# Kernel optimization log

Hardware: AMD Instinct MI355X
Metric: run time of the kernel (lower is better)

Reference implementation:

```python
import jax, jax.numpy as jnp
import numpy as np

IN_FEATURES = 4096
OUT_FEATURES = 768
N_BITS = 8
BATCH = 4096


def setup_inputs() -> dict:
    key = jax.random.key(0)
    k1, k2, k3 = jax.random.split(key, 3)
    latent = jax.random.uniform(k1, (BATCH, IN_FEATURES), dtype=jnp.float32)
    true_sum = jax.random.uniform(k2, (BATCH, OUT_FEATURES * N_BITS), dtype=jnp.float32)
    # kaiming-normal-ish init: std = sqrt(2 / fan_in)
    weight = jax.random.normal(k3, (IN_FEATURES, OUT_FEATURES * N_BITS), dtype=jnp.float32) * np.sqrt(2.0 / IN_FEATURES)
    return {"latent": latent, "true_sum": true_sum, "weight": weight, "n_bits": N_BITS}


def reference(latent, true_sum, weight, n_bits):
    in_features = weight.shape[0]
    batch = latent.shape[0]
    # powers of two, MSB negated (two's-complement style decode)
    powers = (2.0 ** jnp.arange(n_bits, dtype=jnp.float32))
    powers = powers.at[-1].multiply(-1.0)

    prob_weights = jax.nn.sigmoid(weight)                      # [in, out*n_bits]
    # decode soft bits -> integer-valued weights: [in, out]
    int_weights = (prob_weights.reshape(in_features, -1, n_bits) * powers).sum(-1)
    # decode target bits -> integer-valued sums: [batch, out]
    int_sum = (true_sum.reshape(batch, -1, n_bits) * powers).sum(-1)

    # (latent.unsqueeze(-1) * int_weights).sum(-2) is exactly a GEMM
    pred = latent @ int_weights                                # [batch, out]

    scale_factor = 2.0 ** (n_bits - 1)
    recon_loss = jnp.mean((pred - int_sum) ** 2) / scale_factor
    polarize_loss = jnp.mean(prob_weights * (1.0 - prob_weights))
    return (recon_loss, polarize_loss)
```

## Files before the change

### kernel.cpp

```cpp
#include <hip/hip_runtime.h>
#include <stdint.h>

#define IN_F   4096
#define OUT_F  768
#define NB     8
#define BATCH  4096
#define WCOLS  (OUT_F*NB)
#define PREDN  (BATCH*OUT_F)

typedef short  bf16x8  __attribute__((ext_vector_type(8)));
typedef float  f32x4   __attribute__((ext_vector_type(4)));
typedef unsigned short ushort8 __attribute__((ext_vector_type(8)));

__device__ __forceinline__ unsigned short f2bf(float f){
    union { float f; uint32_t u; } v; v.f = f;
    uint32_t u = v.u;
    u += 0x7FFFu + ((u >> 16) & 1u);
    return (unsigned short)(u >> 16);
}

__device__ __forceinline__ void gload16(const void* g, void* l){
    __builtin_amdgcn_global_load_lds(
        (const __attribute__((address_space(1))) unsigned int*)g,
        (__attribute__((address_space(3))) unsigned int*)l, 16, 0, 0);
}

#define SBAR() __builtin_amdgcn_sched_barrier(0)

__launch_bounds__(256)
__global__ void decode_all(const float* __restrict__ w,
                           const float* __restrict__ lat,
                           unsigned short* __restrict__ bt,
                           unsigned short* __restrict__ abf,
                           float* __restrict__ polp){
    __shared__ unsigned short tile[64][70];
    __shared__ float part[4];
    const int tid = threadIdx.x;
    const int bid = blockIdx.x;
    if (bid < 768){
        const int k0 = (bid & 63) * 64;
        const int n0 = (bid >> 6) * 64;
        const int j     = tid & 63;
        const int ibase = (tid >> 6) * 16;
        float pol = 0.f;
        #pragma unroll
        for (int grp = 0; grp < 4; ++grp){
            float4 va[4][2];
            #pragma unroll
            for (int r = 0; r < 4; ++r){
                int i = ibase + grp*4 + r;
                const float4* src = (const float4*)(w + (size_t)(k0+i)*WCOLS
                                                      + (size_t)(n0+j)*8);
                va[r][0] = src[0];
                va[r][1] = src[1];
            }
            SBAR();
            #pragma unroll
            for (int r = 0; r < 4; ++r){
                float x[8] = {va[r][0].x, va[r][0].y, va[r][0].z, va[r][0].w,
                              va[r][1].x, va[r][1].y, va[r][1].z, va[r][1].w};
                float p[8];
                #pragma unroll
                for (int q = 0; q < 8; ++q){
                    p[q] = __builtin_amdgcn_rcpf(1.f + __expf(-x[q]));
                    pol += p[q] * (1.f - p[q]);
                }
                float iw = p[0] + 2.f*p[1] + 4.f*p[2] + 8.f*p[3]
                         + 16.f*p[4] + 32.f*p[5] + 64.f*p[6] - 128.f*p[7];
                tile[j][ibase + grp*4 + r] = f2bf(iw);
            }
        }
        #pragma unroll
        for (int off = 32; off; off >>= 1) pol += __shfl_down(pol, off);
        if ((tid & 63) == 0) part[tid >> 6] = pol;
        __syncthreads();
        const int nrow = tid >> 4;
        const int kb   = (tid & 15) * 4;
        #pragma unroll
        for (int q = 0; q < 4; ++q){
            int n = nrow + q*16;
            uint2 v;
            v.x = *(const unsigned int*)&tile[n][kb];
            v.y = *(const unsigned int*)&tile[n][kb+2];
            *(uint2*)(bt + (size_t)(n0+n)*IN_F + k0 + kb) = v;
        }
        if (tid == 0) polp[bid] = part[0]+part[1]+part[2]+part[3];
    } else {
        const int base = ((bid - 768) * 256 + tid) * 32;
        const float4* p = (const float4*)(lat + base);
        float4 v[8];
        #pragma unroll
        for (int i = 0; i < 8; ++i) v[i] = p[i];
        SBAR();
        #pragma unroll
        for (int h = 0; h < 4; ++h){
            ushort8 o;
            o[0]=f2bf(v[2*h].x);   o[1]=f2bf(v[2*h].y);
            o[2]=f2bf(v[2*h].z);   o[3]=f2bf(v[2*h].w);
            o[4]=f2bf(v[2*h+1].x); o[5]=f2bf(v[2*h+1].y);
            o[6]=f2bf(v[2*h+1].z); o[7]=f2bf(v[2*h+1].w);
            *(ushort8*)(abf + base + h*8) = o;
        }
    }
}

#define BM 128
#define BN 96
#define BK 64
#define NTH 32
#define ABYTES (BM*BK*2)
#define BBYTES (BN*BK*2)
#define BUFB   (ABYTES+BBYTES)

__launch_bounds__(256)
__global__ void gemm_pred(const unsigned short* __restrict__ abf,
                          const unsigned short* __restrict__ bt,
                          float* __restrict__ pred){
    __shared__ __align__(16) char smem[2*BUFB];
    const int tid = threadIdx.x;
    const int w   = tid >> 6;
    const int l   = tid & 63;
    const int s   = l & 15, g = l >> 4;
    const int wr  = w >> 1, wc = w & 1;
    const int bid  = blockIdx.x;
    const int half = bid >> 8;
    const int rem  = bid & 255;
    const int m0   = (rem >> 3) * BM;
    const int n0   = (rem & 7)  * BN;
    const int kb   = half * (NTH*BK);

    f32x4 accv[4][3];
    #pragma unroll
    for (int m = 0; m < 4; ++m)
        #pragma unroll
        for (int n = 0; n < 3; ++n)
            accv[m][n] = (f32x4){0.f,0.f,0.f,0.f};

    const int c8  = tid & 7;
    const int r0  = tid >> 3;
    const int scw = ((c8 ^ (r0 & 7)) << 3);
    const unsigned short* aS = abf + (size_t)(m0 + r0) * IN_F + kb + scw;
    const unsigned short* bS = bt  + (size_t)(n0 + r0) * IN_F + kb + scw;

    #define STAGE(kt, base) do {                                           \
        const int _ko = (kt) * BK;                                         \
        char* _ad = (base) + tid*16;                                       \
        char* _bd = (base) + ABYTES + tid*16;                              \
        _Pragma("unroll")                                                  \
        for (int _i = 0; _i < 4; ++_i)                                     \
            gload16(aS + (size_t)_i*32*IN_F + _ko, _ad + _i*4096);         \
        _Pragma("unroll")                                                  \
        for (int _i = 0; _i < 3; ++_i)                                     \
            gload16(bS + (size_t)_i*32*IN_F + _ko, _bd + _i*4096);         \
    } while (0)

    #define COMPUTE(base) do {                                             \
        char* _Ab = (base);                                                \
        char* _Bb = (base) + ABYTES;                                       \
        _Pragma("unroll")                                                  \
        for (int _kk = 0; _kk < 2; ++_kk){                                 \
            bf16x8 _af[4], _bf[3];                                         \
            _Pragma("unroll")                                              \
            for (int _m = 0; _m < 4; ++_m){                                \
                int _r  = wr*64 + _m*16 + s;                               \
                int _ch = _r*8 + ((_kk*4 + g) ^ (_r & 7));                 \
                _af[_m] = *(const bf16x8*)(_Ab + _ch*16);                  \
            }                                                              \
            _Pragma("unroll")                                              \
            for (int _n = 0; _n < 3; ++_n){                                \
                int _r  = wc*48 + _n*16 + s;                               \
                int _ch = _r*8 + ((_kk*4 + g) ^ (_r & 7));                 \
                _bf[_n] = *(const bf16x8*)(_Bb + _ch*16);                  \
            }                                                              \
            __builtin_amdgcn_s_setprio(1);                                 \
            _Pragma("unroll")                                              \
            for (int _m = 0; _m < 4; ++_m)                                 \
                _Pragma("unroll")                                          \
                for (int _n = 0; _n < 3; ++_n)                             \
                    accv[_m][_n] = __builtin_amdgcn_mfma_f32_16x16x32_bf16(\
                        _af[_m], _bf[_n], accv[_m][_n], 0, 0, 0);          \
            __builtin_amdgcn_s_setprio(0);                                 \
        }                                                                  \
    } while (0)

    char* b0 = smem;
    char* b1 = smem + BUFB;
    STAGE(0, b0);
    __syncthreads();
    for (int t = 0; t < NTH; ++t){
        if (t + 1 < NTH) STAGE(t + 1, (t & 1) ? b0 : b1);
        COMPUTE((t & 1) ? b1 : b0);
        __syncthreads();
    }

    float* slab = pred + (size_t)half * PREDN;
    #pragma unroll
    for (int m = 0; m < 4; ++m){
        int rbase = m0 + wr*64 + m*16 + g*4;
        #pragma unroll
        for (int n = 0; n < 3; ++n){
            int col = n0 + wc*48 + n*16 + s;
            #pragma unroll
            for (int jj = 0; jj < 4; ++jj)
                slab[(size_t)(rbase+jj)*OUT_F + col] = accv[m][n][jj];
        }
    }
}

__launch_bounds__(256)
__global__ void loss_pass(const float* __restrict__ pred,
                          const float* __restrict__ ts,
                          float* __restrict__ lossp){
    __shared__ float part[4];
    const int tid = threadIdx.x;
    const int e0  = (blockIdx.x * 256 + tid) * 4;
    const float4 p0 = *(const float4*)(pred + e0);
    const float4 p1 = *(const float4*)(pred + (size_t)PREDN + e0);
    float4 t[8];
    const float4* r = (const float4*)(ts + (size_t)e0 * 8);
    #pragma unroll
    for (int i = 0; i < 8; ++i) t[i] = r[i];
    SBAR();
    float local = 0.f;
    #pragma unroll
    for (int q = 0; q < 4; ++q){
        float4 x = t[2*q], y = t[2*q+1];
        float is = x.x + 2.f*x.y + 4.f*x.z + 8.f*x.w
                 + 16.f*y.x + 32.f*y.y + 64.f*y.z - 128.f*y.w;
        float pv = (q==0) ? (p0.x+p1.x) : (q==1) ? (p0.y+p1.y)
                 : (q==2) ? (p0.z+p1.z) : (p0.w+p1.w);
        float d = pv - is;
        local += d*d;
    }
    #pragma unroll
    for (int off = 32; off; off >>= 1) local += __shfl_down(local, off);
    if ((tid & 63) == 0) part[tid >> 6] = local;
    __syncthreads();
    if (tid == 0) lossp[blockIdx.x] = part[0]+part[1]+part[2]+part[3];
}

__launch_bounds__(256)
__global__ void finalize(const float* __restrict__ lossp,
                         const float* __restrict__ polp,
                         float* __restrict__ out){
    __shared__ float sm[2][4];
    const int tid = threadIdx.x;
    float a = 0.f, b = 0.f;
    for (int i = tid; i < 3072; i += 256) a += lossp[i];
    for (int i = tid; i < 768;  i += 256) b += polp[i];
    #pragma unroll
    for (int off = 32; off; off >>= 1){
        a += __shfl_down(a, off);
        b += __shfl_down(b, off);
    }
    if ((tid & 63) == 0){ sm[0][tid >> 6] = a; sm[1][tid >> 6] = b; }
    __syncthreads();
    if (tid == 0){
        float sa = sm[0][0]+sm[0][1]+sm[0][2]+sm[0][3];
        float sb = sm[1][0]+sm[1][1]+sm[1][2]+sm[1][3];
        out[0] = sa * (1.0f / ((float)BATCH * (float)OUT_F * 128.0f));
        out[1] = sb * (1.0f / ((float)IN_F * (float)WCOLS));
    }
}

extern "C" void kernel_launch(void* const* d_in, const int* in_sizes, int n_in,
                              void* d_out, int out_size, void* d_ws, size_t ws_size,
                              hipStream_t stream){
    const float* latent   = (const float*)d_in[0];
    const float* true_sum = (const float*)d_in[1];
    const float* weight   = (const float*)d_in[2];
    char* ws = (char*)d_ws;
    float* lossp = (float*)ws;
    float* polp  = (float*)(ws + 32768);
    unsigned short* bt  = (unsigned short*)(ws + 65536);
    unsigned short* abf = (unsigned short*)(ws + 65536 + 6291456);
    float* pred = (float*)(ws + 65536 + 6291456 + 33554432);
    float* out = (float*)d_out;

    decode_all<<<768 + 2048, 256, 0, stream>>>(weight, latent, bt, abf, polp);
    gemm_pred<<<512, 256, 0, stream>>>(abf, bt, pred);
    loss_pass<<<PREDN/1024, 256, 0, stream>>>(pred, true_sum, lossp);
    finalize<<<1, 256, 0, stream>>>(lossp, polp, out);
}
```

Measured before the change: 111.5 us.

## Coalesce global loads in decode and loss kernels via lane-pair bit splitting

Reworks the weight decode, latent conversion and loss kernels so adjacent lanes read adjacent 16-byte chunks, replacing the per-thread 32-byte strided reads. Each lane pair splits the 8 bit-planes into low and high halves, weights them with parity-dependent powers, and combines the halves with a shuffle-xor. In the loss pass both lanes of a pair compute the same squared error, so the sum is halved. The goal is fully coalesced memory transactions in these bandwidth-bound passes, at the cost of extra shuffles and duplicated difference work.

Result: faster. 107.1 us (-3.9%).

```diff
diff --git a/kernel.cpp b/kernel.cpp
--- a/kernel.cpp
+++ b/kernel.cpp
@@ -10,7 +10,7 @@
 
 typedef short  bf16x8  __attribute__((ext_vector_type(8)));
 typedef float  f32x4   __attribute__((ext_vector_type(4)));
-typedef unsigned short ushort8 __attribute__((ext_vector_type(8)));
+typedef unsigned short ushort4v __attribute__((ext_vector_type(4)));
 
 __device__ __forceinline__ unsigned short f2bf(float f){
     union { float f; uint32_t u; } v; v.f = f;
@@ -40,34 +40,41 @@
     if (bid < 768){
         const int k0 = (bid & 63) * 64;
         const int n0 = (bid >> 6) * 64;
-        const int j     = tid & 63;
-        const int ibase = (tid >> 6) * 16;
+        const int wv = tid >> 6;
+        const int l  = tid & 63;
+        const int par = l & 1;
+        const float c0 = par ? 16.f : 1.f;
+        const float c1 = par ? 32.f : 2.f;
+        const float c2 = par ? 64.f : 4.f;
+        const float c3 = par ? -128.f : 8.f;
+        const f32x4* wf4 = (const f32x4*)w;
         float pol = 0.f;
         #pragma unroll
-        for (int grp = 0; grp < 4; ++grp){
-            float4 va[4][2];
+        for (int rq = 0; rq < 4; ++rq){
+            f32x4 va[4][2];
             #pragma unroll
-            for (int r = 0; r < 4; ++r){
-                int i = ibase + grp*4 + r;
-                const float4* src = (const float4*)(w + (size_t)(k0+i)*WCOLS
-                                                      + (size_t)(n0+j)*8);
-                va[r][0] = src[0];
-                va[r][1] = src[1];
+            for (int rr = 0; rr < 4; ++rr){
+                int i = wv*16 + rq*4 + rr;
+                size_t rb = (size_t)(k0 + i) * 1536 + n0 * 2;
+                va[rr][0] = wf4[rb + l];
+                va[rr][1] = wf4[rb + 64 + l];
             }
             SBAR();
             #pragma unroll
-            for (int r = 0; r < 4; ++r){
-                float x[8] = {va[r][0].x, va[r][0].y, va[r][0].z, va[r][0].w,
-                              va[r][1].x, va[r][1].y, va[r][1].z, va[r][1].w};
-                float p[8];
+            for (int rr = 0; rr < 4; ++rr){
+                int i = wv*16 + rq*4 + rr;
                 #pragma unroll
-                for (int q = 0; q < 8; ++q){
-                    p[q] = __builtin_amdgcn_rcpf(1.f + __expf(-x[q]));
-                    pol += p[q] * (1.f - p[q]);
+                for (int h = 0; h < 2; ++h){
+                    f32x4 v = va[rr][h];
+                    float s0 = __builtin_amdgcn_rcpf(1.f + __expf(-v[0]));
+                    float s1 = __builtin_amdgcn_rcpf(1.f + __expf(-v[1]));
+                    float s2 = __builtin_amdgcn_rcpf(1.f + __expf(-v[2]));
+                    float s3 = __builtin_amdgcn_rcpf(1.f + __expf(-v[3]));
+                    pol += s0*(1.f-s0) + s1*(1.f-s1) + s2*(1.f-s2) + s3*(1.f-s3);
+                    float d = s0*c0 + s1*c1 + s2*c2 + s3*c3;
+                    float iw = d + __shfl_xor(d, 1);
+                    tile[h*32 + (l >> 1)][i] = f2bf(iw);
                 }
-                float iw = p[0] + 2.f*p[1] + 4.f*p[2] + 8.f*p[3]
-                         + 16.f*p[4] + 32.f*p[5] + 64.f*p[6] - 128.f*p[7];
-                tile[j][ibase + grp*4 + r] = f2bf(iw);
             }
         }
         #pragma unroll
@@ -86,20 +93,19 @@
         }
         if (tid == 0) polp[bid] = part[0]+part[1]+part[2]+part[3];
     } else {
-        const int base = ((bid - 768) * 256 + tid) * 32;
-        const float4* p = (const float4*)(lat + base);
-        float4 v[8];
-        #pragma unroll
-        for (int i = 0; i < 8; ++i) v[i] = p[i];
+        const int base = (bid - 768) * 8192;
+        const f32x4* p = (const f32x4*)(lat + base);
+        ushort4v* o = (ushort4v*)(abf + base);
+        f32x4 v[8];
+        #pragma unroll
+        for (int i = 0; i < 8; ++i) v[i] = p[tid + i*256];
         SBAR();
         #pragma unroll
-        for (int h = 0; h < 4; ++h){
-            ushort8 o;
-            o[0]=f2bf(v[2*h].x);   o[1]=f2bf(v[2*h].y);
-            o[2]=f2bf(v[2*h].z);   o[3]=f2bf(v[2*h].w);
-            o[4]=f2bf(v[2*h+1].x); o[5]=f2bf(v[2*h+1].y);
-            o[6]=f2bf(v[2*h+1].z); o[7]=f2bf(v[2*h+1].w);
-            *(ushort8*)(abf + base + h*8) = o;
+        for (int i = 0; i < 8; ++i){
+            ushort4v u;
+            u[0]=f2bf(v[i][0]); u[1]=f2bf(v[i][1]);
+            u[2]=f2bf(v[i][2]); u[3]=f2bf(v[i][3]);
+            o[tid + i*256] = u;
         }
     }
 }
@@ -213,30 +219,39 @@
                           float* __restrict__ lossp){
     __shared__ float part[4];
     const int tid = threadIdx.x;
-    const int e0  = (blockIdx.x * 256 + tid) * 4;
-    const float4 p0 = *(const float4*)(pred + e0);
-    const float4 p1 = *(const float4*)(pred + (size_t)PREDN + e0);
-    float4 t[8];
-    const float4* r = (const float4*)(ts + (size_t)e0 * 8);
-    #pragma unroll
-    for (int i = 0; i < 8; ++i) t[i] = r[i];
+    const int blk = blockIdx.x;
+    const f32x4* tsp = (const f32x4*)(ts + (size_t)blk * 8192);
+    const int par = tid & 1;
+    const float c0 = par ? 16.f : 1.f;
+    const float c1 = par ? 32.f : 2.f;
+    const float c2 = par ? 64.f : 4.f;
+    const float c3 = par ? -128.f : 8.f;
+
+    f32x4 v[8];
+    float pr0[8], pr1[8];
+    #pragma unroll
+    for (int i = 0; i < 8; ++i) v[i] = tsp[tid + i*256];
+    #pragma unroll
+    for (int i = 0; i < 8; ++i){
+        int E = blk*1024 + (tid >> 1) + i*128;
+        pr0[i] = pred[E];
+        pr1[i] = pred[(size_t)PREDN + E];
+    }
     SBAR();
     float local = 0.f;
     #pragma unroll
-    for (int q = 0; q < 4; ++q){
-        float4 x = t[2*q], y = t[2*q+1];
-        float is = x.x + 2.f*x.y + 4.f*x.z + 8.f*x.w
-                 + 16.f*y.x + 32.f*y.y + 64.f*y.z - 128.f*y.w;
-        float pv = (q==0) ? (p0.x+p1.x) : (q==1) ? (p0.y+p1.y)
-                 : (q==2) ? (p0.z+p1.z) : (p0.w+p1.w);
-        float d = pv - is;
-        local += d*d;
-    }
+    for (int i = 0; i < 8; ++i){
+        float d = v[i][0]*c0 + v[i][1]*c1 + v[i][2]*c2 + v[i][3]*c3;
+        float is = d + __shfl_xor(d, 1);
+        float diff = (pr0[i] + pr1[i]) - is;
+        local += diff*diff;
+    }
+    local *= 0.5f;
     #pragma unroll
     for (int off = 32; off; off >>= 1) local += __shfl_down(local, off);
     if ((tid & 63) == 0) part[tid >> 6] = local;
     __syncthreads();
-    if (tid == 0) lossp[blockIdx.x] = part[0]+part[1]+part[2]+part[3];
+    if (tid == 0) lossp[blk] = part[0]+part[1]+part[2]+part[3];
 }
 
 __launch_bounds__(256)
```
